# Kernel tuning notes

Measured on AMD Instinct MI355X. Metric: run time of the kernel, lower is better.

Reference implementation:

```python
import jax, jax.numpy as jnp
import numpy as np

SEQ, H, VOCAB = 2048, 1024, 32000

def setup_inputs() -> dict:
    key = jax.random.key(0)
    ks = jax.random.split(key, 13)
    s = lambda k, shape, fan: jax.random.normal(k, shape, dtype=jnp.float32) / np.sqrt(fan)
    return {
        "word_input": jax.random.randint(ks[0], (1,), 0, VOCAB, dtype=jnp.int64),
        "last_context": s(ks[1], (1, H), H),
        "last_hidden": s(ks[2], (1, H), H),
        "encoder_outputs": s(ks[3], (SEQ, H), H),
        "emb": s(ks[4], (VOCAB, H), H),
        "W_ih": s(ks[5], (4 * H, 2 * H), 2 * H),
        "W_hh": s(ks[6], (4 * H, H), H),
        "b_ih": s(ks[7], (4 * H,), H),
        "b_hh": s(ks[8], (4 * H,), H),
        "Wa": s(ks[9], (H, H), H),
        "ba": s(ks[10], (H,), H),
        "Wl": s(ks[11], (VOCAB, 2 * H), 2 * H),
        "bl": s(ks[12], (VOCAB,), 2 * H),
    }

def reference(word_input, last_context, last_hidden, encoder_outputs,
              emb, W_ih, W_hh, b_ih, b_hh, Wa, ba, Wl, bl):
    # embedding lookup (batch=1, single step): [H]
    x = emb[word_input[0]]
    # rnn_input = cat(embedded, last_context): [2H]
    inp = jnp.concatenate([x, last_context[0]])
    h0 = last_hidden[0]
    c0 = jnp.zeros_like(h0)
    # single LSTM step, PyTorch gate order (i, f, g, o)
    gates = W_ih @ inp + b_ih + W_hh @ h0 + b_hh  # [4H]
    i_g, f_g, g_g, o_g = jnp.split(gates, 4)
    c = jax.nn.sigmoid(f_g) * c0 + jax.nn.sigmoid(i_g) * jnp.tanh(g_g)
    h = jax.nn.sigmoid(o_g) * jnp.tanh(c)  # lstm_output, [H]
    # Bahdanau-style scores: dot(h, Wa @ enc_i + ba) for each position (vectorized)
    energies = (encoder_outputs @ Wa.T + ba) @ h  # [SEQ]
    attn_w = jax.nn.softmax(energies)
    context = attn_w @ encoder_outputs  # [H]
    logits = Wl @ jnp.concatenate([h, context]) + bl  # [VOCAB]
    out = jax.nn.log_softmax(logits)
    return out[None, :]  # [1, VOCAB]
```

## Files before the change

### kernel.cpp

```cpp
#include <hip/hip_runtime.h>
#include <hip/hip_bf16.h>
#include <math.h>

#define SEQ   2048
#define H     1024
#define VOCAB 32000
#define GRID2 2048
#define NTHR  256

__device__ inline float4 ld4(const float* p) { return *reinterpret_cast<const float4*>(p); }
__device__ inline float dot4(float4 a, float4 b) { return a.x*b.x + a.y*b.y + a.z*b.z + a.w*b.w; }
__device__ inline float sigmoidf(float x) { return 1.f / (1.f + expf(-x)); }

__device__ inline void omerge(float& m, float& s, float m2, float s2) {
    if (m2 > m) { s = s * __expf(m - m2) + s2; m = m2; }
    else if (s2 != 0.f) { s += s2 * __expf(m2 - m); }
}
__device__ inline float waveSum(float v) {
#pragma unroll
    for (int off = 32; off > 0; off >>= 1) v += __shfl_down(v, off, 64);
    return v;
}
__device__ inline void waveOmerge(float& m, float& s) {
#pragma unroll
    for (int off = 32; off > 0; off >>= 1) {
        float m2 = __shfl_down(m, off, 64), ss = __shfl_down(s, off, 64);
        omerge(m, s, m2, ss);
    }
}

#define SHARDS 16
#define SHSTRIDE 32

__device__ inline void blockSignalSh(unsigned* f) {
    __syncthreads();
    if (threadIdx.x == 0) {
        __threadfence();
        __hip_atomic_fetch_add(&f[(blockIdx.x & (SHARDS - 1)) * SHSTRIDE], 1u,
                               __ATOMIC_RELEASE, __HIP_MEMORY_SCOPE_AGENT);
    }
}
__device__ inline unsigned shSum(unsigned* f) {
    unsigned sum = 0;
#pragma unroll
    for (int q = 0; q < SHARDS; ++q)
        sum += __hip_atomic_load(&f[q * SHSTRIDE], __ATOMIC_RELAXED,
                                 __HIP_MEMORY_SCOPE_AGENT);
    return sum;
}
__device__ inline void blockWaitSlow(unsigned* f, unsigned target) {
    if (threadIdx.x == 0) {
        int it = 0;
        while (shSum(f) < target) {
            if (it < 2)       __builtin_amdgcn_s_sleep(1);
            else if (it < 4)  __builtin_amdgcn_s_sleep(2);
            else if (it < 6)  __builtin_amdgcn_s_sleep(4);
            else if (it < 8)  __builtin_amdgcn_s_sleep(8);
            else if (it < 10) __builtin_amdgcn_s_sleep(16);
            else if (it < 12) __builtin_amdgcn_s_sleep(32);
            else              __builtin_amdgcn_s_sleep(64);
            ++it;
        }
        __threadfence();
    }
    __syncthreads();
}
__device__ inline void blockWaitFast(unsigned* f, unsigned target) {
    if (threadIdx.x == 0) {
        int it = 0;
        while (shSum(f) < target) {
            if (it < 2)      __builtin_amdgcn_s_sleep(1);
            else if (it < 4) __builtin_amdgcn_s_sleep(2);
            else if (it < 6) __builtin_amdgcn_s_sleep(4);
            else             __builtin_amdgcn_s_sleep(8);
            ++it;
        }
        __threadfence();
    }
    __syncthreads();
}


__global__ __launch_bounds__(NTHR) void k_init(float* __restrict__ ws) {
    const int t = threadIdx.x;
    unsigned* fl = (unsigned*)ws;
    for (int k = t; k < 2560; k += NTHR) fl[k] = 0u;
    float* ctx = ws + 3584;
    float* u   = ws + 4608;
    for (int k = t; k < H; k += NTHR) { u[k] = 0.f; ctx[k] = 0.f; }
}

__global__ __launch_bounds__(NTHR, 8) void k_main(
        const float* __restrict__ emb,  const float* __restrict__ lctx,
        const float* __restrict__ h0,   const float* __restrict__ W_ih,
        const float* __restrict__ W_hh, const float* __restrict__ b_ih,
        const float* __restrict__ b_hh, const int* __restrict__ widx,
        const float* __restrict__ enc,  const float* __restrict__ Wa,
        const float* __restrict__ Wl,   const float* __restrict__ bl,
        float* __restrict__ ws, float* __restrict__ out) {
    const int bid = blockIdx.x, t = threadIdx.x;
    const int wid = t >> 6, lane = t & 63;

    unsigned* f_h   = (unsigned*)ws + 0;
    unsigned* f_u   = (unsigned*)ws + 512;
    unsigned* f_e   = (unsigned*)ws + 1024;
    unsigned* f_ctx = (unsigned*)ws + 1536;
    unsigned* f_l   = (unsigned*)ws + 2048;
    float*  vcat   = ws + 2560;
    float*  h      = vcat;
    float*  ctx    = vcat + H;
    float*  u      = ws + 4608;
    float*  energ  = ws + 5632;
    float2* part_e = (float2*)(ws + 7680);
    float2* part_l = (float2*)(ws + 8192);

    __shared__ float  lg[12];
    __shared__ float  shh[16];
    __shared__ float  se[8];
    __shared__ float  shw[32];
    __shared__ float2 s2[4];

    if (bid < 1024) {
        const int j = bid;
        const int w = widx[0];
        const float* xep = emb + (size_t)w * H;
        const float* wi = W_ih + (size_t)j * (2 * H);
        const float* wg = W_ih + (size_t)(j + 2 * H) * (2 * H);
        const float* wo = W_ih + (size_t)(j + 3 * H) * (2 * H);
        const float* vi = W_hh + (size_t)j * H;
        const float* vg = W_hh + (size_t)(j + 2 * H) * H;
        const float* vo = W_hh + (size_t)(j + 3 * H) * H;
        const int e = t * 4;
        float4 x0 = ld4(xep + e), x1 = ld4(lctx + e), x2 = ld4(h0 + e);
        float ai = dot4(ld4(wi + e), x0) + dot4(ld4(wi + H + e), x1) + dot4(ld4(vi + e), x2);
        float ag = dot4(ld4(wg + e), x0) + dot4(ld4(wg + H + e), x1) + dot4(ld4(vg + e), x2);
        float ao = dot4(ld4(wo + e), x0) + dot4(ld4(wo + H + e), x1) + dot4(ld4(vo + e), x2);
        ai = waveSum(ai); ag = waveSum(ag); ao = waveSum(ao);
        if (lane == 0) { lg[wid*3] = ai; lg[wid*3+1] = ag; lg[wid*3+2] = ao; }
        __syncthreads();
        if (t == 0) {
            float gi = 0.f, gg = 0.f, go = 0.f;
            for (int q = 0; q < 4; ++q) { gi += lg[q*3]; gg += lg[q*3+1]; go += lg[q*3+2]; }
            gi += b_ih[j] + b_hh[j];
            gg += b_ih[j + 2*H] + b_hh[j + 2*H];
            go += b_ih[j + 3*H] + b_hh[j + 3*H];
            float c = sigmoidf(gi) * tanhf(gg);
            h[j] = sigmoidf(go) * tanhf(c);
        }
        blockSignalSh(f_h);
    }

    blockWaitSlow(f_h, 1024);

    if (bid >= 1024 && bid < 1280) {
        const int ab = bid - 1024;
        {
            const int rg = ab >> 2, kb = ab & 3;
            if (t < 16) shh[t] = h[rg * 16 + t];
            __syncthreads();
            const int k = kb * 256 + t;
            float acc = 0.f;
#pragma unroll
            for (int jj = 0; jj < 16; ++jj)
                acc += Wa[(size_t)(rg * 16 + jj) * H + k] * shh[jj];
            atomicAdd(&u[k], acc);
            blockSignalSh(f_u);
            blockWaitFast(f_u, 256);
        }
        {
#pragma unroll
            for (int rr = 0; rr < 2; ++rr) {
                const int row = ab * 8 + wid * 2 + rr;
                const float* er = enc + (size_t)row * H;
                float acc = 0.f;
#pragma unroll
                for (int it = 0; it < 4; ++it) {
                    const int e = it * 256 + lane * 4;
                    acc += dot4(ld4(er + e), ld4(u + e));
                }
                acc = waveSum(acc);
                if (lane == 0) { energ[row] = acc; se[wid * 2 + rr] = acc; }
            }
            __syncthreads();
            if (t == 0) {
                float m = -INFINITY, s = 0.f;
                for (int q = 0; q < 8; ++q) omerge(m, s, se[q], 1.f);
                part_e[ab] = make_float2(m, s);
            }
            blockSignalSh(f_e);
            blockWaitFast(f_e, 256);
        }
        {
            float2 p = part_e[t];
            float m = p.x, s = p.y;
            waveOmerge(m, s);
            if (lane == 0) s2[wid] = make_float2(m, s);
            __syncthreads();
            float M = s2[0].x, S = s2[0].y;
#pragma unroll
            for (int q = 1; q < 4; ++q) omerge(M, S, s2[q].x, s2[q].y);
            const float invS = 1.f / S;
            const int rg = ab >> 2, kb = ab & 3;
            __syncthreads();
            if (t < 32) shw[t] = __expf(energ[rg * 32 + t] - M) * invS;
            __syncthreads();
            const int k = kb * 256 + t;
            float acc = 0.f;
#pragma unroll
            for (int jj = 0; jj < 32; ++jj)
                acc += shw[jj] * enc[(size_t)(rg * 32 + jj) * H + k];
            atomicAdd(&ctx[k], acc);
            blockSignalSh(f_ctx);
            blockWaitFast(f_ctx, 256);
        }
        {
            const int aw = ab * 4 + wid;
            float4 xv[8];
#pragma unroll
            for (int q = 0; q < 8; ++q) xv[q] = ld4(vcat + q * 256 + lane * 4);
            float lm = -INFINITY, ls = 0.f;
#pragma unroll
            for (int rr = 0; rr < 4; ++rr) {
                if (rr < 3 || aw < 256) {
                    const int r = 28672 + aw + 1024 * rr;
                    const float* wr = Wl + (size_t)r * (2 * H);
                    float a = 0.f;
#pragma unroll
                    for (int q = 0; q < 8; ++q)
                        a += dot4(ld4(wr + q * 256 + lane * 4), xv[q]);
                    a = waveSum(a);
                    if (lane == 0) {
                        float v = a + bl[r];
                        out[r] = v;
                        omerge(lm, ls, v, 1.f);
                    }
                }
            }
            if (lane == 0) s2[wid] = make_float2(lm, ls);
            __syncthreads();
            if (t == 0) {
                float M = s2[0].x, S = s2[0].y;
#pragma unroll
                for (int q = 1; q < 4; ++q) omerge(M, S, s2[q].x, s2[q].y);
                part_l[bid] = make_float2(M, S);
            }
            blockSignalSh(f_l);
        }
    } else {
        const int sw = (bid < 1024) ? bid * 4 + wid : (bid - 256) * 4 + wid;
        const int r0 = sw * 4;
        float4 xv[4];
#pragma unroll
        for (int q = 0; q < 4; ++q) xv[q] = ld4(h + q * 256 + lane * 4);
        float acc4[4];
#pragma unroll
        for (int rr = 0; rr < 4; ++rr) {
            const float* wr = Wl + (size_t)(r0 + rr) * (2 * H);
            float a = 0.f;
#pragma unroll
            for (int q = 0; q < 4; ++q)
                a += dot4(ld4(wr + q * 256 + lane * 4), xv[q]);
            acc4[rr] = a;
        }
        blockWaitSlow(f_ctx, 256);
#pragma unroll
        for (int q = 0; q < 4; ++q) xv[q] = ld4(ctx + q * 256 + lane * 4);
        float lm = -INFINITY, ls = 0.f;
#pragma unroll
        for (int rr = 0; rr < 4; ++rr) {
            const int r = r0 + rr;
            const float* wr = Wl + (size_t)r * (2 * H) + H;
            float a = acc4[rr];
#pragma unroll
            for (int q = 0; q < 4; ++q)
                a += dot4(ld4(wr + q * 256 + lane * 4), xv[q]);
            a = waveSum(a);
            if (lane == 0) {
                float v = a + bl[r];
                out[r] = v;
                omerge(lm, ls, v, 1.f);
            }
        }
        if (lane == 0) s2[wid] = make_float2(lm, ls);
        __syncthreads();
        if (t == 0) {
            float M = s2[0].x, S = s2[0].y;
#pragma unroll
            for (int q = 1; q < 4; ++q) omerge(M, S, s2[q].x, s2[q].y);
            part_l[bid] = make_float2(M, S);
        }
        blockSignalSh(f_l);
    }

    if (bid < 125) {
        blockWaitSlow(f_l, 2048);
        float m = -INFINITY, s = 0.f;
#pragma unroll
        for (int q = 0; q < 8; ++q) {
            float2 p = part_l[t + q * 256];
            omerge(m, s, p.x, p.y);
        }
        waveOmerge(m, s);
        if (lane == 0) s2[wid] = make_float2(m, s);
        __syncthreads();
        float M = s2[0].x, S = s2[0].y;
#pragma unroll
        for (int q = 1; q < 4; ++q) omerge(M, S, s2[q].x, s2[q].y);
        const float lse = M + logf(S);
        const int i = bid * 256 + t;
        out[i] = out[i] - lse;
    }
}


__global__ __launch_bounds__(256) void k_lstm(
        const float* __restrict__ emb, const float* __restrict__ lctx,
        const float* __restrict__ h0,  const float* __restrict__ W_ih,
        const float* __restrict__ W_hh, const float* __restrict__ b_ih,
        const float* __restrict__ b_hh, const int* __restrict__ widx,
        float* __restrict__ h_out, float* __restrict__ u_zero,
        float* __restrict__ ctx_zero) {
    const int j = blockIdx.x, t = threadIdx.x;
    const int wid = t >> 6, lane = t & 63;
    if (j == 0) for (int k = t; k < H; k += 256) u_zero[k] = 0.f;
    if (j == 1) for (int k = t; k < H; k += 256) ctx_zero[k] = 0.f;
    const int w = widx[0];
    const float* embrow = emb + (size_t)w * H;
    const int ri = j, rg = j + 2 * H, ro = j + 3 * H;
    const float* wi_i = W_ih + (size_t)ri * (2 * H);
    const float* wi_g = W_ih + (size_t)rg * (2 * H);
    const float* wi_o = W_ih + (size_t)ro * (2 * H);
    const float* wh_i = W_hh + (size_t)ri * H;
    const float* wh_g = W_hh + (size_t)rg * H;
    const float* wh_o = W_hh + (size_t)ro * H;
    float ai = 0.f, ag = 0.f, ao = 0.f;
    { int e = t*4; float4 x = ld4(embrow+e);
      ai += dot4(ld4(wi_i+e),x); ag += dot4(ld4(wi_g+e),x); ao += dot4(ld4(wi_o+e),x); }
    { int e = t*4; float4 x = ld4(lctx+e);
      ai += dot4(ld4(wi_i+H+e),x); ag += dot4(ld4(wi_g+H+e),x); ao += dot4(ld4(wi_o+H+e),x); }
    { int e = t*4; float4 x = ld4(h0+e);
      ai += dot4(ld4(wh_i+e),x); ag += dot4(ld4(wh_g+e),x); ao += dot4(ld4(wh_o+e),x); }
    ai = waveSum(ai); ag = waveSum(ag); ao = waveSum(ao);
    __shared__ float lds[12];
    if (lane == 0) { lds[wid*3] = ai; lds[wid*3+1] = ag; lds[wid*3+2] = ao; }
    __syncthreads();
    if (t == 0) {
        float gi = 0.f, gg = 0.f, go = 0.f;
        for (int q = 0; q < 4; ++q) { gi += lds[q*3]; gg += lds[q*3+1]; go += lds[q*3+2]; }
        gi += b_ih[ri] + b_hh[ri];
        gg += b_ih[rg] + b_hh[rg];
        go += b_ih[ro] + b_hh[ro];
        float c = sigmoidf(gi) * tanhf(gg);
        h_out[j] = sigmoidf(go) * tanhf(c);
    }
}

__global__ __launch_bounds__(256) void k_wa(
        const float* __restrict__ Wa, const float* __restrict__ h,
        float* __restrict__ u) {
    const int k = blockIdx.x * 256 + threadIdx.x;
    const int j0 = blockIdx.y * 32;
    float acc = 0.f;
#pragma unroll 8
    for (int j = j0; j < j0 + 32; ++j) acc += Wa[(size_t)j * H + k] * h[j];
    atomicAdd(&u[k], acc);
}

__global__ __launch_bounds__(256) void k_energy(
        const float* __restrict__ enc, const float* __restrict__ u,
        float* __restrict__ energ, float2* __restrict__ part_e) {
    const int t = threadIdx.x, wid = t >> 6, lane = t & 63;
    const int row = blockIdx.x * 4 + wid;
    const float* er = enc + (size_t)row * H;
    float acc = 0.f;
#pragma unroll
    for (int it = 0; it < 4; ++it) { int e = it*256 + lane*4; acc += dot4(ld4(er+e), ld4(u+e)); }
    acc = waveSum(acc);
    __shared__ float se[4];
    if (lane == 0) { energ[row] = acc; se[wid] = acc; }
    __syncthreads();
    if (t == 0) {
        float m = fmaxf(fmaxf(se[0], se[1]), fmaxf(se[2], se[3]));
        float s = __expf(se[0]-m) + __expf(se[1]-m) + __expf(se[2]-m) + __expf(se[3]-m);
        part_e[blockIdx.x] = make_float2(m, s);
    }
}

__global__ __launch_bounds__(256) void k_ctx(
        const float* __restrict__ enc, const float* __restrict__ energ,
        const float2* __restrict__ part_e, float* __restrict__ ctx) {
    const int t = threadIdx.x, wid = t >> 6, lane = t & 63;
    __shared__ float2 s2[4];
    __shared__ float sh[64];
    float2 a = part_e[t], b = part_e[t + 256];
    float m = a.x, s = a.y;
    omerge(m, s, b.x, b.y);
    waveOmerge(m, s);
    if (lane == 0) s2[wid] = make_float2(m, s);
    __syncthreads();
    float M = s2[0].x, S = s2[0].y;
#pragma unroll
    for (int q = 1; q < 4; ++q) omerge(M, S, s2[q].x, s2[q].y);
    const float invS = 1.f / S;
    const int j0 = (blockIdx.x >> 2) * 64;
    __syncthreads();
    if (t < 64) sh[t] = __expf(energ[j0 + t] - M) * invS;
    __syncthreads();
    const int k = (blockIdx.x & 3) * 256 + t;
    float acc = 0.f;
#pragma unroll 8
    for (int jj = 0; jj < 64; ++jj) acc += sh[jj] * enc[(size_t)(j0 + jj) * H + k];
    atomicAdd(&ctx[k], acc);
}

__global__ __launch_bounds__(256) void k_logits(
        const float* __restrict__ Wl, const float* __restrict__ vcat,
        const float* __restrict__ bl, float* __restrict__ logits,
        float2* __restrict__ part_l) {
    const int t = threadIdx.x, wid = t >> 6, lane = t & 63;
    const int gw = blockIdx.x * 4 + wid;
    float4 xv[8];
#pragma unroll
    for (int q = 0; q < 8; ++q) xv[q] = ld4(vcat + q * 256 + lane * 4);
    float lm = -INFINITY, ls = 0.f;
#pragma unroll
    for (int rr = 0; rr < 4; ++rr) {
        const int row = gw * 4 + rr;
        const float* wr = Wl + (size_t)row * (2 * H);
        float acc = 0.f;
#pragma unroll
        for (int q = 0; q < 8; ++q)
            acc += dot4(ld4(wr + q * 256 + lane * 4), xv[q]);
        acc = waveSum(acc);
        if (lane == 0) {
            float v = acc + bl[row];
            logits[row] = v;
            omerge(lm, ls, v, 1.f);
        }
    }
    __shared__ float2 s2[4];
    if (lane == 0) s2[wid] = make_float2(lm, ls);
    __syncthreads();
    if (t == 0) {
        float M = s2[0].x, S = s2[0].y;
#pragma unroll
        for (int q = 1; q < 4; ++q) omerge(M, S, s2[q].x, s2[q].y);
        part_l[blockIdx.x] = make_float2(M, S);
    }
}

__global__ __launch_bounds__(256) void k_final(
        const float* __restrict__ logits, const float2* __restrict__ part_l,
        float* __restrict__ out) {
    const int t = threadIdx.x, wid = t >> 6, lane = t & 63;
    __shared__ float2 s2[4];
    float m = -INFINITY, s = 0.f;
    for (int i = t; i < 2000; i += 256) {
        float2 p = part_l[i];
        omerge(m, s, p.x, p.y);
    }
    waveOmerge(m, s);
    if (lane == 0) s2[wid] = make_float2(m, s);
    __syncthreads();
    float M = s2[0].x, S = s2[0].y;
#pragma unroll
    for (int q = 1; q < 4; ++q) omerge(M, S, s2[q].x, s2[q].y);
    const float lse = M + logf(S);
    const int i = blockIdx.x * 256 + t;
    out[i] = logits[i] - lse;
}

extern "C" void kernel_launch(void* const* d_in, const int* in_sizes, int n_in,
                              void* d_out, int out_size, void* d_ws, size_t ws_size,
                              hipStream_t stream) {
    const int*   widx = (const int*)d_in[0];
    const float* lctx = (const float*)d_in[1];
    const float* h0   = (const float*)d_in[2];
    const float* enc  = (const float*)d_in[3];
    const float* emb  = (const float*)d_in[4];
    const float* W_ih = (const float*)d_in[5];
    const float* W_hh = (const float*)d_in[6];
    const float* b_ih = (const float*)d_in[7];
    const float* b_hh = (const float*)d_in[8];
    const float* Wa   = (const float*)d_in[9];
    const float* Wl   = (const float*)d_in[11];
    const float* bl   = (const float*)d_in[12];
    float* out = (float*)d_out;
    float* ws  = (float*)d_ws;

    int occ = 0, nCU = 0, dev = 0;
    hipGetDevice(&dev);
    hipDeviceGetAttribute(&nCU, hipDeviceAttributeMultiprocessorCount, dev);
    hipError_t oe = hipOccupancyMaxActiveBlocksPerMultiprocessor(
        &occ, (const void*)k_main, NTHR, 0);
    const bool persistent_ok = (oe == hipSuccess) && ((long)occ * nCU >= GRID2);

    if (persistent_ok) {
        k_init<<<1, NTHR, 0, stream>>>(ws);
        k_main<<<GRID2, NTHR, 0, stream>>>(emb, lctx, h0, W_ih, W_hh, b_ih,
                                           b_hh, widx, enc, Wa, Wl, bl, ws, out);
    } else {
        float*  h      = ws;
        float*  ctx    = ws + 1024;
        float*  u      = ws + 2048;
        float*  energ  = ws + 3072;
        float2* part_e = (float2*)(ws + 5120);
        float2* part_l = (float2*)(ws + 6144);
        float*  logits = ws + 10240;
        k_lstm  <<<1024, 256, 0, stream>>>(emb, lctx, h0, W_ih, W_hh, b_ih, b_hh, widx, h, u, ctx);
        k_wa    <<<dim3(4, 32), 256, 0, stream>>>(Wa, h, u);
        k_energy<<<512, 256, 0, stream>>>(enc, u, energ, part_e);
        k_ctx   <<<128, 256, 0, stream>>>(enc, energ, part_e, ctx);
        k_logits<<<2000, 256, 0, stream>>>(Wl, ws , bl, logits, part_l);
        k_final <<<125, 256, 0, stream>>>(logits, part_l, out);
    }
}
```

Measured before the change: 73.29 us.

## Fuse energy and context into one-pass flash-style partials across 512 attention blocks

Attention blocks grow from 256 to 512. Each block now computes four energies, keeps the encoder rows in shared memory, and writes an unnormalized partial context alongside its local max and sum. This replaces the old second pass that reread enc, and drops one grid-wide barrier. The context is then reduced from the 512 partials by column. Logit row assignment changes to 5 rows per wave for the streaming blocks. Blocks no longer all wait on h before starting. This adds a 2MB partial workspace, 16KB of shared memory per block (which may lower occupancy), and a strided column reduction.

```diff
diff --git a/kernel.cpp b/kernel.cpp
--- a/kernel.cpp
+++ b/kernel.cpp
@@ -80,13 +80,14 @@
     __syncthreads();
 }
 
+#define WS_NEED_FLOATS (11008 + 512 * 1024)
 
 __global__ __launch_bounds__(NTHR) void k_init(float* __restrict__ ws) {
     const int t = threadIdx.x;
     unsigned* fl = (unsigned*)ws;
-    for (int k = t; k < 2560; k += NTHR) fl[k] = 0u;
-    float* ctx = ws + 3584;
-    float* u   = ws + 4608;
+    for (int k = t; k < 2816; k += NTHR) fl[k] = 0u;
+    float* ctx = ws + 3840;
+    float* u   = ws + 4864;
     for (int k = t; k < H; k += NTHR) { u[k] = 0.f; ctx[k] = 0.f; }
 }
 
@@ -106,18 +107,18 @@
     unsigned* f_e   = (unsigned*)ws + 1024;
     unsigned* f_ctx = (unsigned*)ws + 1536;
     unsigned* f_l   = (unsigned*)ws + 2048;
-    float*  vcat   = ws + 2560;
+    float*  vcat   = ws + 2816;
     float*  h      = vcat;
     float*  ctx    = vcat + H;
-    float*  u      = ws + 4608;
-    float*  energ  = ws + 5632;
-    float2* part_e = (float2*)(ws + 7680);
-    float2* part_l = (float2*)(ws + 8192);
-
+    float*  u      = ws + 4864;
+    float2* part_e = (float2*)(ws + 5888);
+    float2* part_l = (float2*)(ws + 6912);
+    float*  ctxp   = ws + 11008;
+
+    __shared__ __align__(16) float encS[4][1024];
     __shared__ float  lg[12];
     __shared__ float  shh[16];
     __shared__ float  se[8];
-    __shared__ float  shw[32];
     __shared__ float2 s2[4];
 
     if (bid < 1024) {
@@ -150,11 +151,10 @@
         blockSignalSh(f_h);
     }
 
-    blockWaitSlow(f_h, 1024);
-
-    if (bid >= 1024 && bid < 1280) {
+    if (bid >= 1024 && bid < 1536) {
         const int ab = bid - 1024;
-        {
+        if (ab < 256) {
+            blockWaitFast(f_h, 1024);
             const int rg = ab >> 2, kb = ab & 3;
             if (t < 16) shh[t] = h[rg * 16 + t];
             __syncthreads();
@@ -165,75 +165,82 @@
                 acc += Wa[(size_t)(rg * 16 + jj) * H + k] * shh[jj];
             atomicAdd(&u[k], acc);
             blockSignalSh(f_u);
-            blockWaitFast(f_u, 256);
-        }
+        }
+        blockWaitFast(f_u, 256);
         {
-#pragma unroll
-            for (int rr = 0; rr < 2; ++rr) {
-                const int row = ab * 8 + wid * 2 + rr;
-                const float* er = enc + (size_t)row * H;
-                float acc = 0.f;
-#pragma unroll
-                for (int it = 0; it < 4; ++it) {
-                    const int e = it * 256 + lane * 4;
-                    acc += dot4(ld4(er + e), ld4(u + e));
-                }
-                acc = waveSum(acc);
-                if (lane == 0) { energ[row] = acc; se[wid * 2 + rr] = acc; }
-            }
+            const int r = ab * 4 + wid;
+            const float* er = enc + (size_t)r * H;
+            float acc = 0.f;
+#pragma unroll
+            for (int q = 0; q < 4; ++q) {
+                const int e = q * 256 + lane * 4;
+                float4 ev = ld4(er + e);
+                *(float4*)&encS[wid][e] = ev;
+                acc += dot4(ev, ld4(u + e));
+            }
+            acc = waveSum(acc);
+            if (lane == 0) se[wid] = acc;
             __syncthreads();
+            const float m = fmaxf(fmaxf(se[0], se[1]), fmaxf(se[2], se[3]));
             if (t == 0) {
-                float m = -INFINITY, s = 0.f;
-                for (int q = 0; q < 8; ++q) omerge(m, s, se[q], 1.f);
+                float s = __expf(se[0]-m) + __expf(se[1]-m)
+                        + __expf(se[2]-m) + __expf(se[3]-m);
                 part_e[ab] = make_float2(m, s);
             }
-            blockSignalSh(f_e);
-            blockWaitFast(f_e, 256);
-        }
+            const float w0 = __expf(se[0]-m), w1 = __expf(se[1]-m);
+            const float w2 = __expf(se[2]-m), w3 = __expf(se[3]-m);
+#pragma unroll
+            for (int c = 0; c < 4; ++c) {
+                const int k = c * 256 + t;
+                ctxp[(size_t)ab * 1024 + k] = w0*encS[0][k] + w1*encS[1][k]
+                                            + w2*encS[2][k] + w3*encS[3][k];
+            }
+        }
+        blockSignalSh(f_e);
+        blockWaitFast(f_e, 512);
         {
-            float2 p = part_e[t];
-            float m = p.x, s = p.y;
-            waveOmerge(m, s);
-            if (lane == 0) s2[wid] = make_float2(m, s);
+            float2 pa = part_e[t], pb = part_e[t + 256];
+            float M = pa.x, S = pa.y;
+            omerge(M, S, pb.x, pb.y);
+            waveOmerge(M, S);
+            if (lane == 0) s2[wid] = make_float2(M, S);
             __syncthreads();
-            float M = s2[0].x, S = s2[0].y;
-#pragma unroll
-            for (int q = 1; q < 4; ++q) omerge(M, S, s2[q].x, s2[q].y);
-            const float invS = 1.f / S;
-            const int rg = ab >> 2, kb = ab & 3;
-            __syncthreads();
-            if (t < 32) shw[t] = __expf(energ[rg * 32 + t] - M) * invS;
-            __syncthreads();
-            const int k = kb * 256 + t;
-            float acc = 0.f;
-#pragma unroll
-            for (int jj = 0; jj < 32; ++jj)
-                acc += shw[jj] * enc[(size_t)(rg * 32 + jj) * H + k];
-            atomicAdd(&ctx[k], acc);
-            blockSignalSh(f_ctx);
-            blockWaitFast(f_ctx, 256);
-        }
+            float Mg = s2[0].x, Sg = s2[0].y;
+#pragma unroll
+            for (int q = 1; q < 4; ++q) omerge(Mg, Sg, s2[q].x, s2[q].y);
+            const float invS = 1.f / Sg;
+            const float wb0 = __expf(pa.x - Mg);
+            const float wb1 = __expf(pb.x - Mg);
+#pragma unroll
+            for (int c = 0; c < 2; ++c) {
+                const int k = ab * 2 + c;
+                float p = ctxp[(size_t)t * 1024 + k] * wb0
+                        + ctxp[(size_t)(t + 256) * 1024 + k] * wb1;
+                p = waveSum(p);
+                __syncthreads();
+                if (lane == 0) se[wid] = p;
+                __syncthreads();
+                if (t == 0) ctx[k] = (se[0] + se[1] + se[2] + se[3]) * invS;
+            }
+        }
+        blockSignalSh(f_ctx);
+        blockWaitFast(f_ctx, 512);
         {
             const int aw = ab * 4 + wid;
-            float4 xv[8];
-#pragma unroll
-            for (int q = 0; q < 8; ++q) xv[q] = ld4(vcat + q * 256 + lane * 4);
             float lm = -INFINITY, ls = 0.f;
-#pragma unroll
-            for (int rr = 0; rr < 4; ++rr) {
-                if (rr < 3 || aw < 256) {
-                    const int r = 28672 + aw + 1024 * rr;
-                    const float* wr = Wl + (size_t)r * (2 * H);
-                    float a = 0.f;
-#pragma unroll
-                    for (int q = 0; q < 8; ++q)
-                        a += dot4(ld4(wr + q * 256 + lane * 4), xv[q]);
-                    a = waveSum(a);
-                    if (lane == 0) {
-                        float v = a + bl[r];
-                        out[r] = v;
-                        omerge(lm, ls, v, 1.f);
-                    }
+            if (aw < 1280) {
+                const int r = 30720 + aw;
+                const float* wr = Wl + (size_t)r * (2 * H);
+                float a = 0.f;
+#pragma unroll
+                for (int q = 0; q < 8; ++q)
+                    a += dot4(ld4(wr + q * 256 + lane * 4),
+                              ld4(vcat + q * 256 + lane * 4));
+                a = waveSum(a);
+                if (lane == 0) {
+                    float v = a + bl[r];
+                    out[r] = v;
+                    omerge(lm, ls, v, 1.f);
                 }
             }
             if (lane == 0) s2[wid] = make_float2(lm, ls);
@@ -247,30 +254,32 @@
             blockSignalSh(f_l);
         }
     } else {
-        const int sw = (bid < 1024) ? bid * 4 + wid : (bid - 256) * 4 + wid;
-        const int r0 = sw * 4;
+        const int sw = (bid < 1024) ? bid : bid - 512;
+        const int gw = sw * 4 + wid;
+        const int r0 = gw * 5;
+        blockWaitFast(f_h, 1024);
         float4 xv[4];
 #pragma unroll
         for (int q = 0; q < 4; ++q) xv[q] = ld4(h + q * 256 + lane * 4);
-        float acc4[4];
-#pragma unroll
-        for (int rr = 0; rr < 4; ++rr) {
+        float acc5[5];
+#pragma unroll
+        for (int rr = 0; rr < 5; ++rr) {
             const float* wr = Wl + (size_t)(r0 + rr) * (2 * H);
             float a = 0.f;
 #pragma unroll
             for (int q = 0; q < 4; ++q)
                 a += dot4(ld4(wr + q * 256 + lane * 4), xv[q]);
-            acc4[rr] = a;
-        }
-        blockWaitSlow(f_ctx, 256);
+            acc5[rr] = a;
+        }
+        blockWaitFast(f_ctx, 512);
 #pragma unroll
         for (int q = 0; q < 4; ++q) xv[q] = ld4(ctx + q * 256 + lane * 4);
         float lm = -INFINITY, ls = 0.f;
 #pragma unroll
-        for (int rr = 0; rr < 4; ++rr) {
+        for (int rr = 0; rr < 5; ++rr) {
             const int r = r0 + rr;
             const float* wr = Wl + (size_t)r * (2 * H) + H;
-            float a = acc4[rr];
+            float a = acc5[rr];
 #pragma unroll
             for (int q = 0; q < 4; ++q)
                 a += dot4(ld4(wr + q * 256 + lane * 4), xv[q]);
@@ -493,7 +502,8 @@
     hipDeviceGetAttribute(&nCU, hipDeviceAttributeMultiprocessorCount, dev);
     hipError_t oe = hipOccupancyMaxActiveBlocksPerMultiprocessor(
         &occ, (const void*)k_main, NTHR, 0);
-    const bool persistent_ok = (oe == hipSuccess) && ((long)occ * nCU >= GRID2);
+    const bool persistent_ok = (oe == hipSuccess) && ((long)occ * nCU >= GRID2)
+                             && (ws_size >= (size_t)WS_NEED_FLOATS * 4 + 4096);
 
     if (persistent_ok) {
         k_init<<<1, NTHR, 0, stream>>>(ws);
```

Measured after the change: 73.59 us. No clear change (+0.4%).
